# Kernel tuning notes

Measured on AMD Instinct MI355X. Metric: run time of the kernel, lower is better.

Reference implementation:

```python
import jax, jax.numpy as jnp
import numpy as np

N_HEAD = 16
N_EMBD = 1024
HEAD_DIM = N_EMBD // N_HEAD


def setup_inputs() -> dict:
    key = jax.random.key(0)
    k1, k2, k3 = jax.random.split(key, 3)
    B, T, C = 2, 2048, N_EMBD
    x = jax.random.normal(k1, (B, T, C), dtype=jnp.float32)
    # nn.Linear weights: (out_features, in_features)
    W_attn = jax.random.normal(k2, (3 * C, C), dtype=jnp.float32) * 0.02
    W_proj = jax.random.normal(k3, (C, C), dtype=jnp.float32) * 0.02
    return {"x": x, "W_attn": W_attn, "W_proj": W_proj}


def reference(x, W_attn, W_proj):
    B, T, C = x.shape
    h, hd = N_HEAD, HEAD_DIM
    # c_attn: x @ W^T, then split into q, k, v
    qkv = jnp.einsum('btc,dc->btd', x, W_attn)  # [B, T, 3C]
    q, k, v = jnp.split(qkv, 3, axis=-1)
    # [B, T, C] -> [B, h, T, hd]
    q = q.reshape(B, T, h, hd).transpose(0, 2, 1, 3)
    k = k.reshape(B, T, h, hd).transpose(0, 2, 1, 3)
    v = v.reshape(B, T, h, hd).transpose(0, 2, 1, 3)
    # NOTE: no 1/sqrt(hd) scaling in the original module
    logits = jnp.einsum('bhnk,bhmk->bhnm', q, k)  # [B, h, T, T]
    causal = jnp.tril(jnp.ones((T, T), dtype=bool))  # [T, T]
    logits = jnp.where(causal[None, None, :, :], logits, -jnp.inf)
    weights = jax.nn.softmax(logits, axis=-1)
    O = jnp.einsum('bhnm,bhmv->bhnv', weights, v)  # [B, h, T, hd]
    # Original: einsum('bhnv,hdv->bnd', O, c_proj.weight) with weight viewed as (h, d, v)
    Wp = W_proj.reshape(h, C, hd)
    Y = jnp.einsum('bhnv,hdv->bnd', O, Wp)  # [B, T, C]
    return Y
```

## Files before the change

kernel.cpp:

```cpp
#include <hip/hip_runtime.h>
#include <stdint.h>
#include <math.h>

#define B_    2
#define T_    2048
#define C_    1024
#define H_    16
#define D_    64
#define MTOT  4096
#define NQKV  3072
#define KDIM  1024

#define LOG2E 1.4426950408889634f

typedef short short8 __attribute__((ext_vector_type(8)));
typedef float f32x4  __attribute__((ext_vector_type(4)));

__device__ __forceinline__ uint16_t f2b(float f) {
    union { float f; uint32_t u; } x; x.f = f;
    uint32_t u = x.u;
    return (uint16_t)((u + 0x7FFFu + ((u >> 16) & 1u)) >> 16);
}
__device__ __forceinline__ uint32_t packb2(float a, float b) {
    union { float f; uint32_t u; } x, y; x.f = a; y.f = b;
    return __builtin_amdgcn_perm(y.u + 0x8000u, x.u + 0x8000u, 0x07060302u);
}
__device__ __forceinline__ uint32_t packb2_rne(float a, float b) {
    return (uint32_t)f2b(a) | ((uint32_t)f2b(b) << 16);
}
__device__ __forceinline__ float fexp2(float x) {
#if __has_builtin(__builtin_amdgcn_exp2f)
    return __builtin_amdgcn_exp2f(x);
#else
    return exp2f(x);
#endif
}

__global__ __launch_bounds__(256) void cast_all(const float* __restrict__ x,
                                                const float* __restrict__ wa,
                                                uint16_t* __restrict__ xb,
                                                uint16_t* __restrict__ wab,
                                                int n4x, int n4w) {
    int i = blockIdx.x * blockDim.x + threadIdx.x;
    const float* src; uint16_t* dst; int j;
    if (i < n4x) { src = x; dst = xb; j = i; }
    else { j = i - n4x; if (j >= n4w) return; src = wa; dst = wab; }
    float4 v = ((const float4*)src)[j];
    ushort4 o;
    o.x = f2b(v.x); o.y = f2b(v.y); o.z = f2b(v.z); o.w = f2b(v.w);
    ((ushort4*)dst)[j] = o;
}

__global__ __launch_bounds__(256) void cast_wp(const float* __restrict__ wp,
                                               uint16_t* __restrict__ wt) {
    int i = blockIdx.x * blockDim.x + threadIdx.x;
    int j4 = (i & 255) * 4;
    int d  = i >> 8;
    int h = j4 >> 6, v = j4 & 63;
    float4 val = *(const float4*)(wp + h * 65536 + d * 64 + v);
    ushort4 o;
    o.x = f2b(val.x); o.y = f2b(val.y); o.z = f2b(val.z); o.w = f2b(val.w);
    *(ushort4*)(wt + d * 1024 + j4) = o;
}

__global__ __launch_bounds__(256, 3) void gemm_qkv(const uint16_t* __restrict__ A,
                                                   const uint16_t* __restrict__ Bw,
                                                   uint16_t* __restrict__ qkvb) {
    __shared__ __align__(16) uint16_t As[128 * 64];
    __shared__ __align__(16) uint16_t Bs[128 * 64];

    int tid = threadIdx.x;
    int w = tid >> 6, lane = tid & 63;
    int qd = lane >> 4, ln = lane & 15;
    int lnx = ln & 7;
    int rowBase = blockIdx.y * 128;
    int colBase = blockIdx.x * 128;
    int mw = (w >> 1) * 64, nw = (w & 1) * 64;

    int srow = tid >> 3;
    int pchunk = tid & 7;
    int gchunk = pchunk ^ (srow & 7);

    const uint16_t* ga = A  + (size_t)(rowBase + srow) * KDIM + gchunk * 8;
    const uint16_t* gb = Bw + (size_t)(colBase + srow) * KDIM + gchunk * 8;
    uint16_t* la = &As[srow * 64 + pchunk * 8];
    uint16_t* lb = &Bs[srow * 64 + pchunk * 8];

    short8 pa[4], pb[4];
#pragma unroll
    for (int m = 0; m < 4; m++) {
        pa[m] = *(const short8*)(ga + (size_t)m * 32 * KDIM);
        pb[m] = *(const short8*)(gb + (size_t)m * 32 * KDIM);
    }

    f32x4 acc[4][4] = {};
    for (int s = 0; s < 16; s++) {
#pragma unroll
        for (int m = 0; m < 4; m++) {
            *(short8*)(la + m * 32 * 64) = pa[m];
            *(short8*)(lb + m * 32 * 64) = pb[m];
        }
        __syncthreads();
        if (s < 15) {
            int k0 = (s + 1) * 64;
#pragma unroll
            for (int m = 0; m < 4; m++) {
                pa[m] = *(const short8*)(ga + k0 + (size_t)m * 32 * KDIM);
                pb[m] = *(const short8*)(gb + k0 + (size_t)m * 32 * KDIM);
            }
        }
#pragma unroll
        for (int ks = 0; ks < 2; ks++) {
            int p = (ks * 4 + qd) ^ lnx;
            short8 a[4], b[4];
#pragma unroll
            for (int i = 0; i < 4; i++) {
                a[i] = *(const short8*)&As[(mw + i * 16 + ln) * 64 + p * 8];
                b[i] = *(const short8*)&Bs[(nw + i * 16 + ln) * 64 + p * 8];
            }
#pragma unroll
            for (int i = 0; i < 4; i++)
#pragma unroll
                for (int j = 0; j < 4; j++)
                    acc[i][j] = __builtin_amdgcn_mfma_f32_16x16x32_bf16(a[i], b[j], acc[i][j], 0, 0, 0);
        }
        __syncthreads();
    }

#pragma unroll
    for (int i = 0; i < 4; i++) {
#pragma unroll
        for (int j = 0; j < 4; j++) {
            int gcol = colBase + nw + j * 16 + ln;
            int which = gcol >> 10;
            int rem = gcol & 1023;
            int h = rem >> 6, d = rem & 63;
            float sc = (which == 0) ? LOG2E : 1.0f;
#pragma unroll
            for (int r = 0; r < 4; r++) {
                int grow = rowBase + mw + i * 16 + qd * 4 + r;
                int bb = grow >> 11, t = grow & 2047;
                uint16_t val = f2b(acc[i][j][r] * sc);
                if (which == 2) {
                    qkvb[(size_t)2 * 4194304 + (((size_t)(bb * H_ + h) * D_) + d) * T_ + t] = val;
                } else {
                    qkvb[(size_t)which * 4194304 + (((size_t)(bb * H_ + h) * T_) + t) * D_ + d] = val;
                }
            }
        }
    }
}

__global__ __launch_bounds__(256) void attn(const uint16_t* __restrict__ qkvb,
                                            uint16_t* __restrict__ oc) {
    union ShU {
        uint16_t Pl[4][64][72];
        f32x4 X[2][17][64];
    };
    __shared__ __align__(16) ShU sh;

    int tid = threadIdx.x;
    int w = tid >> 6, lane = tid & 63;
    int qd = lane >> 4, ln = lane & 15;
    int bid = blockIdx.x;
    int qt = 31 - (bid >> 5);
    int bh = bid & 31;
    int qbase = qt * 64;
    int ntiles = qt + 1;

    const uint16_t* Q  = qkvb + (size_t)bh * T_ * D_;
    const uint16_t* K  = Q + 4194304;
    const uint16_t* Vt = qkvb + (size_t)2 * 4194304 + (size_t)bh * D_ * T_;

    short8 bq[4][2];
#pragma unroll
    for (int jq = 0; jq < 4; jq++)
#pragma unroll
        for (int ks = 0; ks < 2; ks++)
            bq[jq][ks] = *(const short8*)(Q + (size_t)(qbase + jq * 16 + ln) * D_ + ks * 32 + qd * 8);

    f32x4 ot[4][4] = {};
    float l_part[4] = {};

    for (int kt = w; kt < ntiles; kt += 4) {
        short8 ak[4][2], av[4][2];
#pragma unroll
        for (int it = 0; it < 4; it++)
#pragma unroll
            for (int ks = 0; ks < 2; ks++)
                ak[it][ks] = *(const short8*)(K + (size_t)(kt * 64 + it * 16 + ln) * D_ + ks * 32 + qd * 8);
#pragma unroll
        for (int id = 0; id < 4; id++)
#pragma unroll
            for (int ks = 0; ks < 2; ks++)
                av[id][ks] = *(const short8*)(Vt + (size_t)(id * 16 + ln) * T_ + kt * 64 + ks * 32 + qd * 8);

        bool diag = (kt == qt);
#pragma unroll
        for (int it = 0; it < 4; it++) {
            f32x4 stt[4] = {};
#pragma unroll
            for (int ks = 0; ks < 2; ks++)
#pragma unroll
                for (int jq = 0; jq < 4; jq++)
                    stt[jq] = __builtin_amdgcn_mfma_f32_16x16x32_bf16(ak[it][ks], bq[jq][ks], stt[jq], 0, 0, 0);
            if (diag) {
#pragma unroll
                for (int jq = 0; jq < 4; jq++)
#pragma unroll
                    for (int r = 0; r < 4; r++) {
                        int t = it * 16 + qd * 4 + r;
                        int q = jq * 16 + ln;
                        if (t > q) stt[jq][r] = -1.0e30f;
                    }
            }
#pragma unroll
            for (int jq = 0; jq < 4; jq++) {
                float p0 = fexp2(stt[jq][0]);
                float p1 = fexp2(stt[jq][1]);
                float p2 = fexp2(stt[jq][2]);
                float p3 = fexp2(stt[jq][3]);
                l_part[jq] += (p0 + p1) + (p2 + p3);
                uint2 pk;
                pk.x = packb2(p0, p1);
                pk.y = packb2(p2, p3);
                *(uint2*)&sh.Pl[w][jq * 16 + ln][it * 16 + qd * 4] = pk;
            }
        }

        short8 bp[4][2];
#pragma unroll
        for (int jq = 0; jq < 4; jq++)
#pragma unroll
            for (int ks = 0; ks < 2; ks++)
                bp[jq][ks] = *(const short8*)&sh.Pl[w][jq * 16 + ln][ks * 32 + qd * 8];

#pragma unroll
        for (int ks = 0; ks < 2; ks++)
#pragma unroll
            for (int id = 0; id < 4; id++)
#pragma unroll
                for (int jq = 0; jq < 4; jq++)
                    ot[id][jq] = __builtin_amdgcn_mfma_f32_16x16x32_bf16(av[id][ks], bp[jq][ks], ot[id][jq], 0, 0, 0);
    }

    f32x4 lp = { l_part[0], l_part[1], l_part[2], l_part[3] };
    __syncthreads();
    if (w >= 2) {
#pragma unroll
        for (int id = 0; id < 4; id++)
#pragma unroll
            for (int jq = 0; jq < 4; jq++)
                sh.X[w - 2][id * 4 + jq][lane] = ot[id][jq];
        sh.X[w - 2][16][lane] = lp;
    }
    __syncthreads();
    if (w < 2) {
#pragma unroll
        for (int id = 0; id < 4; id++)
#pragma unroll
            for (int jq = 0; jq < 4; jq++)
                ot[id][jq] += sh.X[w][id * 4 + jq][lane];
        lp += sh.X[w][16][lane];
    }
    __syncthreads();
    if (w == 1) {
#pragma unroll
        for (int id = 0; id < 4; id++)
#pragma unroll
            for (int jq = 0; jq < 4; jq++)
                sh.X[0][id * 4 + jq][lane] = ot[id][jq];
        sh.X[0][16][lane] = lp;
    }
    __syncthreads();
    if (w == 0) {
#pragma unroll
        for (int id = 0; id < 4; id++)
#pragma unroll
            for (int jq = 0; jq < 4; jq++)
                ot[id][jq] += sh.X[0][id * 4 + jq][lane];
        lp += sh.X[0][16][lane];
        float rl[4];
#pragma unroll
        for (int jq = 0; jq < 4; jq++) {
            float s = lp[jq];
            s += __shfl_xor(s, 16);
            s += __shfl_xor(s, 32);
            rl[jq] = 1.0f / s;
        }
        int b = bh >> 4, h = bh & 15;
#pragma unroll
        for (int id = 0; id < 4; id++)
#pragma unroll
            for (int jq = 0; jq < 4; jq++) {
                float v0 = ot[id][jq][0] * rl[jq];
                float v1 = ot[id][jq][1] * rl[jq];
                float v2 = ot[id][jq][2] * rl[jq];
                float v3 = ot[id][jq][3] * rl[jq];
                uint2 pk;
                pk.x = packb2_rne(v0, v1);
                pk.y = packb2_rne(v2, v3);
                int q = qbase + jq * 16 + ln;
                *(uint2*)&oc[(size_t)(b * T_ + q) * C_ + h * 64 + id * 16 + qd * 4] = pk;
            }
    }
}

__global__ __launch_bounds__(256, 3) void gemm_out(const uint16_t* __restrict__ A,
                                                   const uint16_t* __restrict__ Bw,
                                                   float* __restrict__ out) {
    __shared__ __align__(16) uint16_t As[128 * 64];
    __shared__ __align__(16) uint16_t Bs[64 * 64];

    int tid = threadIdx.x;
    int w = tid >> 6, lane = tid & 63;
    int qd = lane >> 4, ln = lane & 15;
    int lnx = ln & 7;
    int rowBase = blockIdx.y * 128;
    int colBase = blockIdx.x * 64;
    int mw = (w >> 1) * 64, nw = (w & 1) * 32;

    int srow = tid >> 3;
    int pchunk = tid & 7;
    int gchunk = pchunk ^ (srow & 7);

    const uint16_t* ga = A  + (size_t)(rowBase + srow) * KDIM + gchunk * 8;
    const uint16_t* gb = Bw + (size_t)(colBase + srow) * KDIM + gchunk * 8;
    uint16_t* la = &As[srow * 64 + pchunk * 8];
    uint16_t* lb = &Bs[srow * 64 + pchunk * 8];

    short8 pa[4], pb[2];
#pragma unroll
    for (int m = 0; m < 4; m++)
        pa[m] = *(const short8*)(ga + (size_t)m * 32 * KDIM);
#pragma unroll
    for (int m = 0; m < 2; m++)
        pb[m] = *(const short8*)(gb + (size_t)m * 32 * KDIM);

    f32x4 acc[4][2] = {};
    for (int s = 0; s < 16; s++) {
#pragma unroll
        for (int m = 0; m < 4; m++)
            *(short8*)(la + m * 32 * 64) = pa[m];
#pragma unroll
        for (int m = 0; m < 2; m++)
            *(short8*)(lb + m * 32 * 64) = pb[m];
        __syncthreads();
        if (s < 15) {
            int k0 = (s + 1) * 64;
#pragma unroll
            for (int m = 0; m < 4; m++)
                pa[m] = *(const short8*)(ga + k0 + (size_t)m * 32 * KDIM);
#pragma unroll
            for (int m = 0; m < 2; m++)
                pb[m] = *(const short8*)(gb + k0 + (size_t)m * 32 * KDIM);
        }
#pragma unroll
        for (int ks = 0; ks < 2; ks++) {
            int p = (ks * 4 + qd) ^ lnx;
            short8 a[4], b[2];
#pragma unroll
            for (int i = 0; i < 4; i++)
                a[i] = *(const short8*)&As[(mw + i * 16 + ln) * 64 + p * 8];
#pragma unroll
            for (int j = 0; j < 2; j++)
                b[j] = *(const short8*)&Bs[(nw + j * 16 + ln) * 64 + p * 8];
#pragma unroll
            for (int i = 0; i < 4; i++)
#pragma unroll
                for (int j = 0; j < 2; j++)
                    acc[i][j] = __builtin_amdgcn_mfma_f32_16x16x32_bf16(a[i], b[j], acc[i][j], 0, 0, 0);
        }
        __syncthreads();
    }

#pragma unroll
    for (int i = 0; i < 4; i++)
#pragma unroll
        for (int j = 0; j < 2; j++)
#pragma unroll
            for (int r = 0; r < 4; r++) {
                int grow = rowBase + mw + i * 16 + qd * 4 + r;
                int gcol = colBase + nw + j * 16 + ln;
                out[(size_t)grow * 1024 + gcol] = acc[i][j][r];
            }
}

extern "C" void kernel_launch(void* const* d_in, const int* in_sizes, int n_in,
                              void* d_out, int out_size, void* d_ws, size_t ws_size,
                              hipStream_t stream) {
    const float* x  = (const float*)d_in[0];
    const float* Wa = (const float*)d_in[1];
    const float* Wp = (const float*)d_in[2];
    float* out = (float*)d_out;

    uint16_t* ws   = (uint16_t*)d_ws;
    uint16_t* xb   = ws;
    uint16_t* Wab  = xb + 4194304;
    uint16_t* Wtb  = Wab + 3145728;
    uint16_t* qkvb = Wtb + 1048576;
    uint16_t* ob   = qkvb + (size_t)3 * 4194304;

    cast_all<<<7168, 256, 0, stream>>>(x, Wa, xb, Wab, 4194304 / 4, 3145728 / 4);
    cast_wp<<<1024, 256, 0, stream>>>(Wp, Wtb);
    gemm_qkv<<<dim3(24, 32), 256, 0, stream>>>(xb, Wab, qkvb);
    attn<<<1024, 256, 0, stream>>>(qkvb, ob);
    gemm_out<<<dim3(16, 32), 256, 0, stream>>>(ob, Wtb, out);
}
```

Before: 184.4 us.

## Software-pipeline K/V loads and split score computation in attention loop

Prefetches the next K tile into registers during the current iteration and delays the V load until after half the score tiles are computed. The P-tile reads from LDS for the first k-half are issued before the second half of QK^T MFMAs, so global and LDS latency can overlap with compute. This raises register pressure (extra live K prefetch registers), which could reduce occupancy.

```diff
diff --git a/kernel.cpp b/kernel.cpp
--- a/kernel.cpp
+++ b/kernel.cpp
@@ -182,22 +182,20 @@
     f32x4 ot[4][4] = {};
     float l_part[4] = {};
 
+    short8 ak[4][2];
+    if (w < ntiles) {
+#pragma unroll
+        for (int it = 0; it < 4; it++)
+#pragma unroll
+            for (int ks = 0; ks < 2; ks++)
+                ak[it][ks] = *(const short8*)(K + (size_t)(w * 64 + it * 16 + ln) * D_ + ks * 32 + qd * 8);
+    }
+
     for (int kt = w; kt < ntiles; kt += 4) {
-        short8 ak[4][2], av[4][2];
-#pragma unroll
-        for (int it = 0; it < 4; it++)
-#pragma unroll
-            for (int ks = 0; ks < 2; ks++)
-                ak[it][ks] = *(const short8*)(K + (size_t)(kt * 64 + it * 16 + ln) * D_ + ks * 32 + qd * 8);
-#pragma unroll
-        for (int id = 0; id < 4; id++)
-#pragma unroll
-            for (int ks = 0; ks < 2; ks++)
-                av[id][ks] = *(const short8*)(Vt + (size_t)(id * 16 + ln) * T_ + kt * 64 + ks * 32 + qd * 8);
-
         bool diag = (kt == qt);
-#pragma unroll
-        for (int it = 0; it < 4; it++) {
+
+#pragma unroll
+        for (int it = 0; it < 2; it++) {
             f32x4 stt[4] = {};
 #pragma unroll
             for (int ks = 0; ks < 2; ks++)
@@ -228,20 +226,73 @@
             }
         }
 
-        short8 bp[4][2];
+        short8 av[4][2];
+#pragma unroll
+        for (int id = 0; id < 4; id++)
+#pragma unroll
+            for (int ks = 0; ks < 2; ks++)
+                av[id][ks] = *(const short8*)(Vt + (size_t)(id * 16 + ln) * T_ + kt * 64 + ks * 32 + qd * 8);
+
+        short8 bp0[4];
 #pragma unroll
         for (int jq = 0; jq < 4; jq++)
+            bp0[jq] = *(const short8*)&sh.Pl[w][jq * 16 + ln][qd * 8];
+
+#pragma unroll
+        for (int it = 2; it < 4; it++) {
+            f32x4 stt[4] = {};
 #pragma unroll
             for (int ks = 0; ks < 2; ks++)
-                bp[jq][ks] = *(const short8*)&sh.Pl[w][jq * 16 + ln][ks * 32 + qd * 8];
-
-#pragma unroll
-        for (int ks = 0; ks < 2; ks++)
-#pragma unroll
-            for (int id = 0; id < 4; id++)
 #pragma unroll
                 for (int jq = 0; jq < 4; jq++)
-                    ot[id][jq] = __builtin_amdgcn_mfma_f32_16x16x32_bf16(av[id][ks], bp[jq][ks], ot[id][jq], 0, 0, 0);
+                    stt[jq] = __builtin_amdgcn_mfma_f32_16x16x32_bf16(ak[it][ks], bq[jq][ks], stt[jq], 0, 0, 0);
+            if (diag) {
+#pragma unroll
+                for (int jq = 0; jq < 4; jq++)
+#pragma unroll
+                    for (int r = 0; r < 4; r++) {
+                        int t = it * 16 + qd * 4 + r;
+                        int q = jq * 16 + ln;
+                        if (t > q) stt[jq][r] = -1.0e30f;
+                    }
+            }
+#pragma unroll
+            for (int jq = 0; jq < 4; jq++) {
+                float p0 = fexp2(stt[jq][0]);
+                float p1 = fexp2(stt[jq][1]);
+                float p2 = fexp2(stt[jq][2]);
+                float p3 = fexp2(stt[jq][3]);
+                l_part[jq] += (p0 + p1) + (p2 + p3);
+                uint2 pk;
+                pk.x = packb2(p0, p1);
+                pk.y = packb2(p2, p3);
+                *(uint2*)&sh.Pl[w][jq * 16 + ln][it * 16 + qd * 4] = pk;
+            }
+        }
+
+        if (kt + 4 < ntiles) {
+#pragma unroll
+            for (int it = 0; it < 4; it++)
+#pragma unroll
+                for (int ks = 0; ks < 2; ks++)
+                    ak[it][ks] = *(const short8*)(K + (size_t)((kt + 4) * 64 + it * 16 + ln) * D_ + ks * 32 + qd * 8);
+        }
+
+        short8 bp1[4];
+#pragma unroll
+        for (int jq = 0; jq < 4; jq++)
+            bp1[jq] = *(const short8*)&sh.Pl[w][jq * 16 + ln][32 + qd * 8];
+
+#pragma unroll
+        for (int id = 0; id < 4; id++)
+#pragma unroll
+            for (int jq = 0; jq < 4; jq++)
+                ot[id][jq] = __builtin_amdgcn_mfma_f32_16x16x32_bf16(av[id][0], bp0[jq], ot[id][jq], 0, 0, 0);
+#pragma unroll
+        for (int id = 0; id < 4; id++)
+#pragma unroll
+            for (int jq = 0; jq < 4; jq++)
+                ot[id][jq] = __builtin_amdgcn_mfma_f32_16x16x32_bf16(av[id][1], bp1[jq], ot[id][jq], 0, 0, 0);
     }
 
     f32x4 lp = { l_part[0], l_part[1], l_part[2], l_part[3] };
```

After: 188.2 us. 2.1% more time.
